# Performance work log

Hardware: AMD Instinct MI355X
Metric: run time of the kernel (lower is better)

## Reference

```python
import jax, jax.numpy as jnp
import numpy as np

N = 2048          # num nodes
F = 64            # in_channels (features)
H = 32            # hidden_channels
O = 32            # out_channels


def setup_inputs() -> dict:
    key = jax.random.key(0)
    ks = jax.random.split(key, 16)
    s = 0.1  # weight scale
    x = jax.random.normal(ks[0], (N, F), jnp.float32)
    # hop-distance-like positive values
    node_distances = jax.random.uniform(ks[1], (N, N), jnp.float32) * 5.0
    # normalization counts; keep away from zero to avoid blowup in division
    normalization_matrix = jax.random.uniform(ks[2], (N, N), jnp.float32) + 1.0
    return {
        "x": x,
        "node_distances": node_distances,
        "normalization_matrix": normalization_matrix,
        # per-feature MLPs f_k: 1 -> H -> H -> O (stacked over F features)
        "fW1": jax.random.normal(ks[3], (F, 1, H), jnp.float32) * s,
        "fb1": jnp.zeros((F, H), jnp.float32),
        "fW2": jax.random.normal(ks[4], (F, H, H), jnp.float32) * s,
        "fb2": jnp.zeros((F, H), jnp.float32),
        "fW3": jax.random.normal(ks[5], (F, H, O), jnp.float32) * s,
        "fb3": jnp.zeros((F, O), jnp.float32),
        # rho MLP: 1 -> H -> H -> 1
        "rW1": jax.random.normal(ks[6], (1, H), jnp.float32) * s,
        "rb1": jnp.zeros((H,), jnp.float32),
        "rW2": jax.random.normal(ks[7], (H, H), jnp.float32) * s,
        "rb2": jnp.zeros((H,), jnp.float32),
        "rW3": jax.random.normal(ks[8], (H, 1), jnp.float32) * s,
        "rb3": jnp.zeros((1,), jnp.float32),
    }


def _f_sums(x, fW1, fb1, fW2, fb2, fW3, fb3):
    # per-feature scalar MLP applied to every entry of x, then summed over features
    h = jax.nn.relu(x[:, :, None] * fW1[None, :, 0, :] + fb1)       # [N,F,H]
    h = jax.nn.relu(jnp.einsum('nfh,fhg->nfg', h, fW2) + fb2)       # [N,F,H]
    fx = jnp.einsum('nfh,fho->nfo', h, fW3) + fb3                   # [N,F,O]
    return fx.sum(axis=1)                                           # [N,O]


def _rho(d, rW1, rb1, rW2, rb2, rW3, rb3):
    # scalar MLP 1 -> H -> H -> 1 applied elementwise to distance matrix d [N,N]
    h = jax.nn.relu(d[..., None] * rW1[0] + rb1)                    # [N,N,H]
    h = jax.nn.relu(jnp.einsum('nmh,hg->nmg', h, rW2) + rb2)        # [N,N,H]
    return jnp.einsum('nmh,ho->nmo', h, rW3)[..., 0] + rb3[0]       # [N,N]


def reference(x, node_distances, normalization_matrix,
              fW1, fb1, fW2, fb2, fW3, fb3,
              rW1, rb1, rW2, rb2, rW3, rb3):
    f_sums = _f_sums(x, fW1, fb1, fW2, fb2, fW3, fb3)               # [N,O]
    rho_d = _rho(node_distances, rW1, rb1, rW2, rb2, rW3, rb3)      # [N,N]
    rho_d = rho_d / normalization_matrix                            # normalize_rho=True
    # pred[node] = sum_m rho_d[node, m] * f_sums[m]
    return rho_d @ f_sums                                            # [N,O]
```

## Files before the change

### kernel.cpp

```cpp
#include <hip/hip_runtime.h>

#define NN 2048
#define FF 64
#define HH 32
#define OO 32

#define WS_FSUMS 0
#define WS_QPOS  262144
#define WS_QNEG  270336
#define WS_QB    278528
#define WS_CPR   278656
#define WS_FLAGS 278664

__global__ __launch_bounds__(256) void precompute_all_kernel(
    const float* __restrict__ fW1, const float* __restrict__ fb1,
    const float* __restrict__ fW2, const float* __restrict__ fb2,
    const float* __restrict__ fW3, const float* __restrict__ fb3,
    const float* __restrict__ rW1, const float* __restrict__ rb1,
    const float* __restrict__ rW2, const float* __restrict__ rb2,
    const float* __restrict__ rW3,
    float* __restrict__ q_pos, float* __restrict__ q_neg,
    float* __restrict__ qb, float* __restrict__ cpr,
    int* __restrict__ flags, float* __restrict__ out)
{
    __shared__ float sA[HH * HH];
    __shared__ float sB[FF * OO];
    __shared__ float sC[128];
    __shared__ int sflags[2];

    const int t = threadIdx.x;

    if (blockIdx.x < FF) {
        const int f = blockIdx.x;
        ((float4*)out)[blockIdx.x * 256 + t] =
            make_float4(0.f, 0.f, 0.f, 0.f);
        ((float4*)sA)[t] = ((const float4*)&fW2[f * HH * HH])[t];
        ((float4*)sB)[t] = ((const float4*)&fW3[f * HH * OO])[t];
        if (t < HH) sC[64 + t] = fW1[f * HH + t];
        __syncthreads();

        if (t < 64) {
            const int s = t >> 5;
            const int g = t & 31;
            float v = 0.f;
#pragma unroll
            for (int h = 0; h < HH; ++h) {
                const float w1 = sC[64 + h];
                const float a = s ? fminf(w1, 0.f) : fmaxf(w1, 0.f);
                v = fmaf(a, sA[h * HH + g], v);
            }
            sC[t] = s ? fminf(v, 0.f) : fmaxf(v, 0.f);
        }
        __syncthreads();
        if (t < 64) {
            const int s = t >> 5;
            const int o = t & 31;
            float q = 0.f;
#pragma unroll
            for (int g = 0; g < HH; ++g)
                q = fmaf(sC[s * 32 + g], sB[g * OO + o], q);
            if (s) q_neg[f * OO + o] = q;
            else   q_pos[f * OO + o] = q;
        }
        return;
    }

    if (t == 0) { sflags[0] = 1; sflags[1] = 1; }
    ((float4*)sA)[t] = ((const float4*)rW2)[t];
    ((float4*)sB)[t] = ((const float4*)fb3)[t];
    ((float4*)sB)[t + 256] = ((const float4*)fb3)[t + 256];
    if (t < HH) sC[64 + t] = rW1[t];
    else if (t < 64) sC[96 + (t - HH)] = rW3[t - HH];
    __syncthreads();

    if (t < 64) {
        const int s = t >> 5;
        const int g = t & 31;
        float v = 0.f;
#pragma unroll
        for (int h = 0; h < HH; ++h) {
            const float w1 = sC[64 + h];
            const float a = s ? fminf(w1, 0.f) : fmaxf(w1, 0.f);
            v = fmaf(a, sA[h * HH + g], v);
        }
        sC[t] = s ? fminf(v, 0.f) : fmaxf(v, 0.f);
    } else if (t < 96) {
        const int o = t - 64;
        float a = 0.f;
#pragma unroll
        for (int f = 0; f < FF; ++f) a += sB[f * OO + o];
        qb[o] = a;
    } else if (t < 160) {
        const int i = t - 96;
        bool bad;
        if (i < HH) bad = (rb1[i] != 0.f);
        else        bad = (rb2[i - HH] != 0.f);
        if (bad) sflags[1] = 0;
    } else {
        const float4* b1 = (const float4*)fb1;
        const float4* b2 = (const float4*)fb2;
        bool bad = false;
        for (int i = t - 160; i < (FF * HH) / 4; i += 96) {
            const float4 a = b1[i], b = b2[i];
            bad |= (a.x != 0.f) | (a.y != 0.f) | (a.z != 0.f) | (a.w != 0.f);
            bad |= (b.x != 0.f) | (b.y != 0.f) | (b.z != 0.f) | (b.w != 0.f);
        }
        if (bad) sflags[0] = 0;
    }
    __syncthreads();

    if (t < 2) {
        float c = 0.f;
#pragma unroll
        for (int g = 0; g < HH; ++g)
            c = fmaf(sC[t * 32 + g], sC[96 + g], c);
        cpr[t] = c;
    }
    if (t == 0) { flags[0] = sflags[0]; flags[1] = sflags[1]; }
}

__global__ __launch_bounds__(256) void fsums_all_kernel(
    const float* __restrict__ x,
    const float* __restrict__ q_pos, const float* __restrict__ q_neg,
    const float* __restrict__ qb,
    const float* __restrict__ fW1, const float* __restrict__ fb1,
    const float* __restrict__ fW2, const float* __restrict__ fb2,
    const float* __restrict__ fW3, const float* __restrict__ fb3,
    const int* __restrict__ flags,
    float* __restrict__ f_sums)
{
    const int t = threadIdx.x;
    const int n0 = blockIdx.x * 8;

    if (flags[0]) {
        __shared__ float qs[2][FF * OO];
        __shared__ float xs[8 * FF];
        ((float4*)qs[0])[t]       = ((const float4*)q_pos)[t];
        ((float4*)qs[0])[t + 256] = ((const float4*)q_pos)[t + 256];
        ((float4*)qs[1])[t]       = ((const float4*)q_neg)[t];
        ((float4*)qs[1])[t + 256] = ((const float4*)q_neg)[t + 256];
        if (t < 128) ((float4*)xs)[t] = ((const float4*)&x[n0 * FF])[t];
        __syncthreads();

        const int r = t >> 5;
        const int o = t & 31;
        float acc = qb[o];
#pragma unroll
        for (int f = 0; f < FF; ++f) {
            const float xv = xs[r * FF + f];
            const float qv = (xv >= 0.f) ? qs[0][f * OO + o]
                                         : qs[1][f * OO + o];
            acc = fmaf(xv, qv, acc);
        }
        f_sums[(n0 + r) * OO + o] = acc;
        return;
    }

    const int wave = t >> 6;
    const int lane = t & 63;
    for (int pass = 0; pass < 2; ++pass) {
        const int n = n0 + pass * 4 + wave;
        const int f = lane;
        const float xv = x[n * FF + f];

        float h1[HH];
#pragma unroll
        for (int h = 0; h < HH; ++h)
            h1[h] = fmaxf(xv * fW1[f * HH + h] + fb1[f * HH + h], 0.f);

        float h2[HH];
#pragma unroll
        for (int g = 0; g < HH; ++g) h2[g] = fb2[f * HH + g];
#pragma unroll
        for (int h = 0; h < HH; ++h) {
            const float a = h1[h];
            const float* __restrict__ w = &fW2[(f * HH + h) * HH];
#pragma unroll
            for (int g = 0; g < HH; ++g) h2[g] += a * w[g];
        }
#pragma unroll
        for (int g = 0; g < HH; ++g) h2[g] = fmaxf(h2[g], 0.f);

        float acc[OO];
#pragma unroll
        for (int o = 0; o < OO; ++o) acc[o] = fb3[f * OO + o];
#pragma unroll
        for (int h = 0; h < HH; ++h) {
            const float a = h2[h];
            const float* __restrict__ w = &fW3[(f * HH + h) * OO];
#pragma unroll
            for (int o = 0; o < OO; ++o) acc[o] += a * w[o];
        }

#pragma unroll
        for (int o = 0; o < OO; ++o) {
            float v = acc[o];
#pragma unroll
            for (int off = 32; off >= 1; off >>= 1)
                v += __shfl_xor(v, off, 64);
            acc[o] = v;
        }
        if (lane == 0) {
#pragma unroll
            for (int o = 0; o < OO; ++o)
                f_sums[n * OO + o] = acc[o];
        }
    }
}

__global__ __launch_bounds__(256) void rho_all_kernel(
    const float* __restrict__ dmat, const float* __restrict__ norm,
    const float* __restrict__ f_sums,
    const float* __restrict__ cpr, const float* __restrict__ rb3,
    const float* __restrict__ rW1, const float* __restrict__ rb1,
    const float* __restrict__ rW2, const float* __restrict__ rb2,
    const float* __restrict__ rW3,
    const int* __restrict__ flags,
    float* __restrict__ out)
{
    const int t = threadIdx.x;

    if (flags[1]) {
        __shared__ float Bt[128 * 66];
        __shared__ float fsL[128 * 32];

        const int rt = blockIdx.x >> 4;
        const int kb = blockIdx.x & 15;
        const int n0 = rt * 64;
        const int m0 = kb * 128;

        const float cp = cpr[0], cn = cpr[1], b3 = rb3[0];

        {
            const float4* src = (const float4*)&f_sums[m0 * OO];
            float4* dst = (float4*)fsL;
#pragma unroll
            for (int i = 0; i < 4; ++i)
                dst[i * 256 + t] = src[i * 256 + t];
        }

#pragma unroll
        for (int it = 0; it < 8; ++it) {
            const int idx4 = it * 256 + t;
            const int r = idx4 >> 5;
            const int j4 = (idx4 & 31) * 4;
            const long g = (long)(n0 + r) * NN + (m0 + j4);
            const float4 d4 = *(const float4*)&dmat[g];
            const float4 n4 = *(const float4*)&norm[g];
            Bt[(j4 + 0) * 66 + r] =
                fmaf(d4.x >= 0.f ? cp : cn, d4.x, b3) / n4.x;
            Bt[(j4 + 1) * 66 + r] =
                fmaf(d4.y >= 0.f ? cp : cn, d4.y, b3) / n4.y;
            Bt[(j4 + 2) * 66 + r] =
                fmaf(d4.z >= 0.f ? cp : cn, d4.z, b3) / n4.z;
            Bt[(j4 + 3) * 66 + r] =
                fmaf(d4.w >= 0.f ? cp : cn, d4.w, b3) / n4.w;
        }
        __syncthreads();

        const int oq = t & 7;
        const int rg = t >> 3;
        const int r0 = rg * 2;

        float4 acc0 = make_float4(0.f, 0.f, 0.f, 0.f);
        float4 acc1 = make_float4(0.f, 0.f, 0.f, 0.f);

#pragma unroll 4
        for (int j = 0; j < 128; ++j) {
            const float2 b  = *(const float2*)&Bt[j * 66 + r0];
            const float4 fv = *(const float4*)&fsL[j * 32 + oq * 4];
            acc0.x = fmaf(b.x, fv.x, acc0.x);
            acc0.y = fmaf(b.x, fv.y, acc0.y);
            acc0.z = fmaf(b.x, fv.z, acc0.z);
            acc0.w = fmaf(b.x, fv.w, acc0.w);
            acc1.x = fmaf(b.y, fv.x, acc1.x);
            acc1.y = fmaf(b.y, fv.y, acc1.y);
            acc1.z = fmaf(b.y, fv.z, acc1.z);
            acc1.w = fmaf(b.y, fv.w, acc1.w);
        }

        float* p = &out[(n0 + r0) * OO + oq * 4];
        atomicAdd(p + 0, acc0.x);
        atomicAdd(p + 1, acc0.y);
        atomicAdd(p + 2, acc0.z);
        atomicAdd(p + 3, acc0.w);
        atomicAdd(p + OO + 0, acc1.x);
        atomicAdd(p + OO + 1, acc1.y);
        atomicAdd(p + OO + 2, acc1.z);
        atomicAdd(p + OO + 3, acc1.w);
        return;
    }

    __shared__ float red[4][OO];
    const int wave = t >> 6;
    const int lane = t & 63;

    for (int rr = 0; rr < 4; ++rr) {
        const int n = blockIdx.x * 4 + rr;

        float acc[OO];
#pragma unroll
        for (int o = 0; o < OO; ++o) acc[o] = 0.f;

#pragma unroll 1
        for (int m0 = 0; m0 < NN; m0 += 256) {
            const int m = m0 + t;
            const float d = dmat[(long)n * NN + m];

            float h1[HH];
#pragma unroll
            for (int h = 0; h < HH; ++h)
                h1[h] = fmaxf(d * rW1[h] + rb1[h], 0.f);

            float h2[HH];
#pragma unroll
            for (int g = 0; g < HH; ++g) h2[g] = rb2[g];
#pragma unroll
            for (int h = 0; h < HH; ++h) {
                const float a = h1[h];
#pragma unroll
                for (int g = 0; g < HH; ++g) h2[g] += a * rW2[h * HH + g];
            }

            float r = rb3[0];
#pragma unroll
            for (int h = 0; h < HH; ++h)
                r += fmaxf(h2[h], 0.f) * rW3[h];

            r /= norm[(long)n * NN + m];

            const float* __restrict__ fs = &f_sums[m * OO];
#pragma unroll
            for (int o = 0; o < OO; ++o) acc[o] += r * fs[o];
        }

#pragma unroll
        for (int o = 0; o < OO; ++o) {
            float v = acc[o];
#pragma unroll
            for (int off = 32; off >= 1; off >>= 1)
                v += __shfl_xor(v, off, 64);
            acc[o] = v;
        }
        if (lane == 0) {
#pragma unroll
            for (int o = 0; o < OO; ++o) red[wave][o] = acc[o];
        }
        __syncthreads();
        if (t < OO)
            out[n * OO + t] = red[0][t] + red[1][t] + red[2][t] + red[3][t];
        __syncthreads();
    }
}

extern "C" void kernel_launch(void* const* d_in, const int* in_sizes, int n_in,
                              void* d_out, int out_size, void* d_ws, size_t ws_size,
                              hipStream_t stream) {
    const float* x    = (const float*)d_in[0];
    const float* dmat = (const float*)d_in[1];
    const float* norm = (const float*)d_in[2];
    const float* fW1  = (const float*)d_in[3];
    const float* fb1  = (const float*)d_in[4];
    const float* fW2  = (const float*)d_in[5];
    const float* fb2  = (const float*)d_in[6];
    const float* fW3  = (const float*)d_in[7];
    const float* fb3  = (const float*)d_in[8];
    const float* rW1  = (const float*)d_in[9];
    const float* rb1  = (const float*)d_in[10];
    const float* rW2  = (const float*)d_in[11];
    const float* rb2  = (const float*)d_in[12];
    const float* rW3  = (const float*)d_in[13];
    const float* rb3  = (const float*)d_in[14];

    char* ws = (char*)d_ws;
    float* f_sums = (float*)(ws + WS_FSUMS);
    float* q_pos  = (float*)(ws + WS_QPOS);
    float* q_neg  = (float*)(ws + WS_QNEG);
    float* qb     = (float*)(ws + WS_QB);
    float* cpr    = (float*)(ws + WS_CPR);
    int*   flags  = (int*)(ws + WS_FLAGS);

    float* out = (float*)d_out;

    precompute_all_kernel<<<FF + 1, 256, 0, stream>>>(
        fW1, fb1, fW2, fb2, fW3, fb3, rW1, rb1, rW2, rb2, rW3,
        q_pos, q_neg, qb, cpr, flags, out);

    fsums_all_kernel<<<NN / 8, 256, 0, stream>>>(
        x, q_pos, q_neg, qb, fW1, fb1, fW2, fb2, fW3, fb3, flags, f_sums);

    rho_all_kernel<<<512, 256, 0, stream>>>(
        dmat, norm, f_sums, cpr, rb3, rW1, rb1, rW2, rb2, rW3, flags, out);
}
```

Measured before the change: 128.0 us.

## Fuse weight precompute and f_sums kernels using a grid-wide spin barrier

```diff
diff --git a/kernel.cpp b/kernel.cpp
--- a/kernel.cpp
+++ b/kernel.cpp
@@ -11,8 +11,12 @@
 #define WS_QB    278528
 #define WS_CPR   278656
 #define WS_FLAGS 278664
-
-__global__ __launch_bounds__(256) void precompute_all_kernel(
+#define WS_BAR   278672
+
+#define MAGIC 0x13579BDFu
+
+__global__ __launch_bounds__(256) void fused_pre_fsums_kernel(
+    const float* __restrict__ x,
     const float* __restrict__ fW1, const float* __restrict__ fb1,
     const float* __restrict__ fW2, const float* __restrict__ fb2,
     const float* __restrict__ fW3, const float* __restrict__ fb3,
@@ -21,21 +25,27 @@
     const float* __restrict__ rW3,
     float* __restrict__ q_pos, float* __restrict__ q_neg,
     float* __restrict__ qb, float* __restrict__ cpr,
-    int* __restrict__ flags, float* __restrict__ out)
+    int* __restrict__ flags, unsigned* __restrict__ bar,
+    float* __restrict__ f_sums, float* __restrict__ out)
 {
     __shared__ float sA[HH * HH];
     __shared__ float sB[FF * OO];
     __shared__ float sC[128];
+    __shared__ float qs[2][FF * OO];
+    __shared__ float xs[8 * FF];
     __shared__ int sflags[2];
 
     const int t = threadIdx.x;
-
-    if (blockIdx.x < FF) {
-        const int f = blockIdx.x;
-        ((float4*)out)[blockIdx.x * 256 + t] =
-            make_float4(0.f, 0.f, 0.f, 0.f);
+    const int b = blockIdx.x;
+
+    if (t < 64)
+        ((float4*)out)[b * 64 + t] = make_float4(0.f, 0.f, 0.f, 0.f);
+
+    if (b < FF) {
+        const int f = b;
         ((float4*)sA)[t] = ((const float4*)&fW2[f * HH * HH])[t];
-        ((float4*)sB)[t] = ((const float4*)&fW3[f * HH * OO])[t];
+        if (t < 256) ((float4*)sB)[t & 255] =
+            ((const float4*)&fW3[f * HH * OO])[t & 255];
         if (t < HH) sC[64 + t] = fW1[f * HH + t];
         __syncthreads();
 
@@ -62,79 +72,83 @@
             if (s) q_neg[f * OO + o] = q;
             else   q_pos[f * OO + o] = q;
         }
-        return;
-    }
-
-    if (t == 0) { sflags[0] = 1; sflags[1] = 1; }
-    ((float4*)sA)[t] = ((const float4*)rW2)[t];
-    ((float4*)sB)[t] = ((const float4*)fb3)[t];
-    ((float4*)sB)[t + 256] = ((const float4*)fb3)[t + 256];
-    if (t < HH) sC[64 + t] = rW1[t];
-    else if (t < 64) sC[96 + (t - HH)] = rW3[t - HH];
+        __syncthreads();
+        if (t == 0) {
+            __threadfence();
+            __hip_atomic_store(&bar[f], MAGIC, __ATOMIC_RELEASE,
+                               __HIP_MEMORY_SCOPE_AGENT);
+        }
+    } else if (b == FF) {
+        if (t == 0) { sflags[0] = 1; sflags[1] = 1; }
+        ((float4*)sA)[t] = ((const float4*)rW2)[t];
+        ((float4*)sB)[t] = ((const float4*)fb3)[t];
+        ((float4*)sB)[t + 256] = ((const float4*)fb3)[t + 256];
+        if (t < HH) sC[64 + t] = rW1[t];
+        else if (t < 64) sC[96 + (t - HH)] = rW3[t - HH];
+        __syncthreads();
+
+        if (t < 64) {
+            const int s = t >> 5;
+            const int g = t & 31;
+            float v = 0.f;
+#pragma unroll
+            for (int h = 0; h < HH; ++h) {
+                const float w1 = sC[64 + h];
+                const float a = s ? fminf(w1, 0.f) : fmaxf(w1, 0.f);
+                v = fmaf(a, sA[h * HH + g], v);
+            }
+            sC[t] = s ? fminf(v, 0.f) : fmaxf(v, 0.f);
+        } else if (t < 96) {
+            const int o = t - 64;
+            float a = 0.f;
+#pragma unroll
+            for (int f = 0; f < FF; ++f) a += sB[f * OO + o];
+            qb[o] = a;
+        } else if (t < 160) {
+            const int i = t - 96;
+            bool bad;
+            if (i < HH) bad = (rb1[i] != 0.f);
+            else        bad = (rb2[i - HH] != 0.f);
+            if (bad) sflags[1] = 0;
+        } else {
+            const float4* b1 = (const float4*)fb1;
+            const float4* b2 = (const float4*)fb2;
+            bool bad = false;
+            for (int i = t - 160; i < (FF * HH) / 4; i += 96) {
+                const float4 a4 = b1[i], b4 = b2[i];
+                bad |= (a4.x != 0.f) | (a4.y != 0.f) |
+                       (a4.z != 0.f) | (a4.w != 0.f);
+                bad |= (b4.x != 0.f) | (b4.y != 0.f) |
+                       (b4.z != 0.f) | (b4.w != 0.f);
+            }
+            if (bad) sflags[0] = 0;
+        }
+        __syncthreads();
+
+        if (t < 2) {
+            float c = 0.f;
+#pragma unroll
+            for (int g = 0; g < HH; ++g)
+                c = fmaf(sC[t * 32 + g], sC[96 + g], c);
+            cpr[t] = c;
+        }
+        if (t == 0) {
+            flags[0] = sflags[0]; flags[1] = sflags[1];
+            __threadfence();
+            __hip_atomic_store(&bar[FF], MAGIC, __ATOMIC_RELEASE,
+                               __HIP_MEMORY_SCOPE_AGENT);
+        }
+    }
+
+    if (t < FF + 1) {
+        while (__hip_atomic_load(&bar[t], __ATOMIC_ACQUIRE,
+                                 __HIP_MEMORY_SCOPE_AGENT) != MAGIC) {}
+    }
     __syncthreads();
 
-    if (t < 64) {
-        const int s = t >> 5;
-        const int g = t & 31;
-        float v = 0.f;
-#pragma unroll
-        for (int h = 0; h < HH; ++h) {
-            const float w1 = sC[64 + h];
-            const float a = s ? fminf(w1, 0.f) : fmaxf(w1, 0.f);
-            v = fmaf(a, sA[h * HH + g], v);
-        }
-        sC[t] = s ? fminf(v, 0.f) : fmaxf(v, 0.f);
-    } else if (t < 96) {
-        const int o = t - 64;
-        float a = 0.f;
-#pragma unroll
-        for (int f = 0; f < FF; ++f) a += sB[f * OO + o];
-        qb[o] = a;
-    } else if (t < 160) {
-        const int i = t - 96;
-        bool bad;
-        if (i < HH) bad = (rb1[i] != 0.f);
-        else        bad = (rb2[i - HH] != 0.f);
-        if (bad) sflags[1] = 0;
-    } else {
-        const float4* b1 = (const float4*)fb1;
-        const float4* b2 = (const float4*)fb2;
-        bool bad = false;
-        for (int i = t - 160; i < (FF * HH) / 4; i += 96) {
-            const float4 a = b1[i], b = b2[i];
-            bad |= (a.x != 0.f) | (a.y != 0.f) | (a.z != 0.f) | (a.w != 0.f);
-            bad |= (b.x != 0.f) | (b.y != 0.f) | (b.z != 0.f) | (b.w != 0.f);
-        }
-        if (bad) sflags[0] = 0;
-    }
-    __syncthreads();
-
-    if (t < 2) {
-        float c = 0.f;
-#pragma unroll
-        for (int g = 0; g < HH; ++g)
-            c = fmaf(sC[t * 32 + g], sC[96 + g], c);
-        cpr[t] = c;
-    }
-    if (t == 0) { flags[0] = sflags[0]; flags[1] = sflags[1]; }
-}
-
-__global__ __launch_bounds__(256) void fsums_all_kernel(
-    const float* __restrict__ x,
-    const float* __restrict__ q_pos, const float* __restrict__ q_neg,
-    const float* __restrict__ qb,
-    const float* __restrict__ fW1, const float* __restrict__ fb1,
-    const float* __restrict__ fW2, const float* __restrict__ fb2,
-    const float* __restrict__ fW3, const float* __restrict__ fb3,
-    const int* __restrict__ flags,
-    float* __restrict__ f_sums)
-{
-    const int t = threadIdx.x;
-    const int n0 = blockIdx.x * 8;
+    const int n0 = b * 8;
 
     if (flags[0]) {
-        __shared__ float qs[2][FF * OO];
-        __shared__ float xs[8 * FF];
         ((float4*)qs[0])[t]       = ((const float4*)q_pos)[t];
         ((float4*)qs[0])[t + 256] = ((const float4*)q_pos)[t + 256];
         ((float4*)qs[1])[t]       = ((const float4*)q_neg)[t];
@@ -373,21 +387,19 @@
     const float* rb3  = (const float*)d_in[14];
 
     char* ws = (char*)d_ws;
-    float* f_sums = (float*)(ws + WS_FSUMS);
-    float* q_pos  = (float*)(ws + WS_QPOS);
-    float* q_neg  = (float*)(ws + WS_QNEG);
-    float* qb     = (float*)(ws + WS_QB);
-    float* cpr    = (float*)(ws + WS_CPR);
-    int*   flags  = (int*)(ws + WS_FLAGS);
+    float*    f_sums = (float*)(ws + WS_FSUMS);
+    float*    q_pos  = (float*)(ws + WS_QPOS);
+    float*    q_neg  = (float*)(ws + WS_QNEG);
+    float*    qb     = (float*)(ws + WS_QB);
+    float*    cpr    = (float*)(ws + WS_CPR);
+    int*      flags  = (int*)(ws + WS_FLAGS);
+    unsigned* bar    = (unsigned*)(ws + WS_BAR);
 
     float* out = (float*)d_out;
 
-    precompute_all_kernel<<<FF + 1, 256, 0, stream>>>(
-        fW1, fb1, fW2, fb2, fW3, fb3, rW1, rb1, rW2, rb2, rW3,
-        q_pos, q_neg, qb, cpr, flags, out);
-
-    fsums_all_kernel<<<NN / 8, 256, 0, stream>>>(
-        x, q_pos, q_neg, qb, fW1, fb1, fW2, fb2, fW3, fb3, flags, f_sums);
+    fused_pre_fsums_kernel<<<NN / 8, 256, 0, stream>>>(
+        x, fW1, fb1, fW2, fb2, fW3, fb3, rW1, rb1, rW2, rb2, rW3,
+        q_pos, q_neg, qb, cpr, flags, bar, f_sums, out);
 
     rho_all_kernel<<<512, 256, 0, stream>>>(
         dmat, norm, f_sums, cpr, rb3, rW1, rb1, rW2, rb2, rW3, flags, out);
```

New measurement: 148.4 us. 1.16x slower.
